# Kernel optimization log

Measured on AMD Instinct MI355X. Metric: run time of the kernel, lower is better.

The kernel has to match this reference:

```python
import jax, jax.numpy as jnp
import numpy as np
from jax import lax

NMS_RADIUS = 4
THRESHOLD = 0.005
BORDER = 4
MAX_KP = 1024


def _max_pool(x, r):
    # torch max_pool2d pads with -inf; reduce_window 'SAME' pads with init value.
    w = 2 * r + 1
    return lax.reduce_window(x, -jnp.inf, lax.max, (1, w, w), (1, 1, 1), 'SAME')


def simple_nms(scores, radius):
    zeros = jnp.zeros_like(scores)
    max_mask = scores == _max_pool(scores, radius)
    for _ in range(2):
        supp_mask = _max_pool(max_mask.astype(scores.dtype), radius) > 0
        supp_scores = jnp.where(supp_mask, zeros, scores)
        new_max_mask = supp_scores == _max_pool(supp_scores, radius)
        max_mask = max_mask | (new_max_mask & ~supp_mask)
    return jnp.where(max_mask, scores, zeros)


def sample_descriptors(kp, desc, s):
    """Bilinear grid_sample (align_corners=True, zero padding) + L2 normalize.
    kp: [B,N,2] (x,y) full-resolution pixel coords; desc: [B,C,h,w]."""
    b, c, h, w = desc.shape
    k = kp - s / 2 + 0.5
    gx = k[..., 0] / (w * s - 1) * 2.0 - 1.0
    gy = k[..., 1] / (h * s - 1) * 2.0 - 1.0
    x = (gx + 1.0) * 0.5 * (w - 1)  # align_corners=True mapping
    y = (gy + 1.0) * 0.5 * (h - 1)
    x0 = jnp.floor(x); y0 = jnp.floor(y)
    wx1 = x - x0; wy1 = y - y0
    x0i = x0.astype(jnp.int32); y0i = y0.astype(jnp.int32)

    def tap(d_b, xi, yi):  # d_b [C,h,w]; xi,yi [N] -> [C,N], zero outside
        v = ((xi >= 0) & (xi < w) & (yi >= 0) & (yi < h)).astype(d_b.dtype)
        g = d_b[:, jnp.clip(yi, 0, h - 1), jnp.clip(xi, 0, w - 1)]
        return g * v

    def one(d_b, x0i, y0i, wx1, wy1):
        wx0 = 1.0 - wx1; wy0 = 1.0 - wy1
        return (tap(d_b, x0i, y0i) * (wx0 * wy0)
                + tap(d_b, x0i + 1, y0i) * (wx1 * wy0)
                + tap(d_b, x0i, y0i + 1) * (wx0 * wy1)
                + tap(d_b, x0i + 1, y0i + 1) * (wx1 * wy1))

    out = jax.vmap(one)(desc, x0i, y0i, wx1, wy1)  # [B,C,N]
    n = jnp.maximum(jnp.linalg.norm(out, axis=1, keepdims=True), 1e-12)
    return out / n


def conv1x1(w, b, x):  # Conv1d kernel_size=1: [O,I] @ [B,I,N]
    return jnp.einsum('oi,bin->bon', w, x) + b[None, :, None]


def setup_inputs() -> dict:
    key = jax.random.key(0)
    ks = jax.random.split(key, 13)
    B, H, W = 4, 480, 640
    inp = {
        'scores': jax.random.uniform(ks[0], (B, H, W), jnp.float32),
        'd1': jax.random.normal(ks[1], (B, 64, H // 2, W // 2), jnp.float32),
        'd2': jax.random.normal(ks[2], (B, 128, H // 4, W // 4), jnp.float32),
        'cDa': jax.random.normal(ks[3], (B, 256, H // 8, W // 8), jnp.float32),
        'd4': jax.random.normal(ks[4], (B, 256, H // 16, W // 16), jnp.float32),
        'lin0_w': jax.random.normal(ks[5], (256, 256), jnp.float32) / np.sqrt(256),
        'lin0_b': jax.random.normal(ks[6], (256,), jnp.float32) * 0.01,
        'lin1_w': jax.random.normal(ks[7], (128, 128), jnp.float32) / np.sqrt(128),
        'lin1_b': jax.random.normal(ks[8], (128,), jnp.float32) * 0.01,
        'lin2_w': jax.random.normal(ks[9], (64, 64), jnp.float32) / np.sqrt(64),
        'lin2_b': jax.random.normal(ks[10], (64,), jnp.float32) * 0.01,
        'merge_w': jax.random.normal(ks[11], (256, 704), jnp.float32) / np.sqrt(704),
        'merge_b': jax.random.normal(ks[12], (256,), jnp.float32) * 0.01,
    }
    return inp


def reference(scores, d1, d2, cDa, d4, lin0_w, lin0_b, lin1_w, lin1_b,
              lin2_w, lin2_b, merge_w, merge_b):
    B, H, W = scores.shape
    s = simple_nms(scores, NMS_RADIUS)
    ys, xs = jnp.meshgrid(jnp.arange(H), jnp.arange(W), indexing='ij')
    valid = (ys >= BORDER) & (ys < H - BORDER) & (xs >= BORDER) & (xs < W - BORDER)
    masked = jnp.where(valid[None] & (s > THRESHOLD), s, -1.0)
    top_scores, idx = lax.top_k(masked.reshape(B, -1), MAX_KP)
    kx = (idx % W).astype(jnp.float32)
    ky = (idx // W).astype(jnp.float32)
    kp = jnp.stack([kx, ky], axis=-1)  # [B,K,2] (x,y), i.e. torch.flip(k,[1])
    de1 = sample_descriptors(kp, d1, 2)    # [B,64,K]
    de2 = sample_descriptors(kp, d2, 4)    # [B,128,K]
    de3 = sample_descriptors(kp, cDa, 8)   # [B,256,K]
    de4 = sample_descriptors(kp, d4, 16)   # [B,256,K]
    de4 = conv1x1(lin0_w, lin0_b, de4)
    de2 = conv1x1(lin1_w, lin1_b, de2)
    de1 = conv1x1(lin2_w, lin2_b, de1)
    descriptors = conv1x1(merge_w, merge_b,
                          jnp.concatenate([de1, de2, de3, de4], axis=1))
    return kp, top_scores, descriptors
```

## Files before the change

### kernel.cpp

```cpp
#include <hip/hip_runtime.h>
#include <hip/hip_bf16.h>

#define B 4
#define H 480
#define W 640
#define HW (H*W)
#define BHW (B*H*W)
#define NKP 1024
#define THRESH 0.005f
#define CAP 16384
#define NCOL (B*NKP)
#define KTOT 704
#define KPB 4

typedef __attribute__((ext_vector_type(8))) short s8v;
typedef __attribute__((ext_vector_type(4))) float f4v;
typedef struct { float x, y; } __attribute__((aligned(4))) f2u;

__device__ __forceinline__ short f2bf(float f) {
    __hip_bfloat16 h = __float2bfloat16(f);
    return *(short*)&h;
}

__device__ __forceinline__ float max3f(float a, float b, float c) {
    return fmaxf(fmaxf(a, b), c);
}
#define MAX9(A, base, str) \
    max3f(max3f((A)[(base)], (A)[(base)+(str)], (A)[(base)+2*(str)]), \
          max3f((A)[(base)+3*(str)], (A)[(base)+4*(str)], (A)[(base)+5*(str)]), \
          max3f((A)[(base)+6*(str)], (A)[(base)+7*(str)], (A)[(base)+8*(str)]))

__global__ void fuse_all(const float* __restrict__ merge_w, const float* __restrict__ merge_b,
                         const float* __restrict__ lin0_w, const float* __restrict__ lin0_b,
                         const float* __restrict__ lin1_w, const float* __restrict__ lin1_b,
                         const float* __restrict__ lin2_w, const float* __restrict__ lin2_b,
                         short* __restrict__ Mw, float* __restrict__ biasf, int* __restrict__ cnt) {
    if (blockIdx.x == 704) {
        int o = threadIdx.x;
        if (o < 4) cnt[o * 64] = 0;
        float acc = merge_b[o];
        for (int k = 0; k < 64; ++k)  acc += merge_w[o * KTOT + k] * lin2_b[k];
        for (int k = 0; k < 128; ++k) acc += merge_w[o * KTOT + 64 + k] * lin1_b[k];
        for (int k = 0; k < 256; ++k) acc += merge_w[o * KTOT + 448 + k] * lin0_b[k];
        biasf[o] = acc;
        return;
    }
    int e = blockIdx.x * 256 + threadIdx.x;
    int o = e / KTOT;
    int j = e - o * KTOT;
    float acc = 0.0f;
    if (j < 64) {
        for (int k = 0; k < 64; ++k) acc += merge_w[o * KTOT + k] * lin2_w[k * 64 + j];
    } else if (j < 192) {
        int jj = j - 64;
        for (int k = 0; k < 128; ++k) acc += merge_w[o * KTOT + 64 + k] * lin1_w[k * 128 + jj];
    } else if (j < 448) {
        acc = merge_w[o * KTOT + j];
    } else {
        int jj = j - 448;
        for (int k = 0; k < 256; ++k) acc += merge_w[o * KTOT + 448 + k] * lin0_w[k * 256 + jj];
    }
    Mw[o * KTOT + j] = f2bf(acc);
}

__global__ __launch_bounds__(256) void nms1(const float* __restrict__ scores,
                                            float* __restrict__ mask) {
    __shared__ float tile[40][40];
    __shared__ float hm[40][32];
    int bz = blockIdx.z;
    int x0 = blockIdx.x * 32, y0 = blockIdx.y * 32;
    const float* sp = scores + bz * HW;
    for (int t = threadIdx.x; t < 1600; t += 256) {
        int ly = t / 40, lx = t - ly * 40;
        int gy = y0 - 4 + ly, gx = x0 - 4 + lx;
        tile[ly][lx] = (gy >= 0 && gy < H && gx >= 0 && gx < W) ? sp[gy * W + gx] : -INFINITY;
    }
    __syncthreads();
    for (int t = threadIdx.x; t < 1280; t += 256) {
        int ly = t >> 5, lx = t & 31;
        hm[ly][lx] = MAX9(&tile[ly][0], lx, 1);
    }
    __syncthreads();
    for (int t = threadIdx.x; t < 1024; t += 256) {
        int ly = t >> 5, lx = t & 31;
        float m = MAX9(&hm[0][0], ly * 32 + lx, 32);
        float s = tile[ly + 4][lx + 4];
        mask[bz * HW + (y0 + ly) * W + x0 + lx] = (s == m) ? 1.0f : 0.0f;
    }
}

__global__ __launch_bounds__(512) void nms2_compact(const float* __restrict__ scores,
                                                    const float* __restrict__ mask0,
                                                    unsigned long long* __restrict__ cand,
                                                    int* __restrict__ cnt) {
    __shared__ float Sm[56 * 56];
    __shared__ float Mm[64 * 64];
    __shared__ float Zm[56 * 56];
    __shared__ float Tm[64 * 56];
    __shared__ int lcnt, gbase;
    int bz = blockIdx.z;
    int x0 = blockIdx.x * 32, y0 = blockIdx.y * 32;
    const float* sp = scores + bz * HW;
    const float* mp = mask0 + bz * HW;
    if (threadIdx.x == 0) lcnt = 0;
    for (int t = threadIdx.x; t < 4096; t += 512) {
        int ly = t >> 6, lx = t & 63;
        int gy = y0 - 16 + ly, gx = x0 - 16 + lx;
        Mm[t] = (gy >= 0 && gy < H && gx >= 0 && gx < W) ? mp[gy * W + gx] : 0.0f;
    }
    for (int t = threadIdx.x; t < 3136; t += 512) {
        int i = t / 56, j = t - i * 56;
        int gy = y0 - 12 + i, gx = x0 - 12 + j;
        Sm[t] = (gy >= 0 && gy < H && gx >= 0 && gx < W) ? sp[gy * W + gx] : -1.0f;
    }
    __syncthreads();
    for (int t = threadIdx.x; t < 3584; t += 512) {
        int i = t / 56, c = t - i * 56;
        Tm[i * 56 + c] = MAX9(Mm, i * 64 + c, 1);
    }
    __syncthreads();
    for (int t = threadIdx.x; t < 3136; t += 512) {
        int i = t / 56, c = t - i * 56;
        float m = MAX9(Tm, i * 56 + c, 56);
        Zm[t] = (m > 0.0f) ? -1.0f : Sm[t];
    }
    __syncthreads();
    for (int t = threadIdx.x; t < 2688; t += 512) {
        int i = t / 48, c = t - i * 48;
        Tm[i * 56 + c] = MAX9(Zm, i * 56 + c, 1);
    }
    __syncthreads();
    for (int t = threadIdx.x; t < 2304; t += 512) {
        int r = t / 48, c = t - r * 48;
        float m = MAX9(Tm, r * 56 + c, 56);
        float Zc = Zm[(r + 4) * 56 + c + 4];
        int mi = (r + 8) * 64 + c + 8;
        bool nm = (Zc == m) && (Zc >= 0.0f);
        Mm[mi] = (Mm[mi] != 0.0f || nm) ? 1.0f : 0.0f;
    }
    __syncthreads();
    for (int t = threadIdx.x; t < 1920; t += 512) {
        int r = t / 40, c = t - r * 40;
        Tm[r * 56 + c] = MAX9(Mm, (r + 8) * 64 + c + 8, 1);
    }
    __syncthreads();
    for (int t = threadIdx.x; t < 1600; t += 512) {
        int r = t / 40, c = t - r * 40;
        float m = MAX9(Tm, r * 56 + c, 56);
        int zi = (r + 8) * 56 + c + 8;
        Zm[zi] = (m > 0.0f) ? -1.0f : Sm[zi];
    }
    __syncthreads();
    for (int t = threadIdx.x; t < 1280; t += 512) {
        int r = t / 32, c = t & 31;
        Tm[r * 56 + c] = MAX9(Zm, (r + 8) * 56 + c + 8, 1);
    }
    __syncthreads();
    unsigned long long keys[2];
    int nl = 0;
    #pragma unroll
    for (int q = 0; q < 2; ++q) {
        int t = threadIdx.x + q * 512;
        int r3 = t >> 5, c = t & 31;
        float m = MAX9(Tm, r3 * 56 + c, 56);
        float Zc = Zm[(r3 + 12) * 56 + c + 12];
        bool fin = (Mm[(r3 + 16) * 64 + c + 16] != 0.0f) || ((Zc == m) && (Zc >= 0.0f));
        int gy = y0 + r3, gx = x0 + c;
        float sc = Sm[(r3 + 12) * 56 + c + 12];
        if (fin && gy >= 4 && gy < H - 4 && gx >= 4 && gx < W - 4 && sc > THRESH) {
            unsigned r = (unsigned)(gy * W + gx);
            unsigned bits = __float_as_uint(sc) | 0x80000000u;
            keys[nl++] = ((unsigned long long)bits << 32) |
                         (unsigned long long)(0xFFFFFFFFu - r);
        }
    }
    int lpos = 0;
    if (nl) lpos = atomicAdd(&lcnt, nl);
    __syncthreads();
    if (threadIdx.x == 0) gbase = (lcnt > 0) ? atomicAdd(&cnt[bz * 64], lcnt) : 0;
    __syncthreads();
    for (int j = 0; j < nl; ++j) {
        int p = gbase + lpos + j;
        if (p < CAP) cand[(size_t)bz * CAP + p] = keys[j];
    }
}

__global__ __launch_bounds__(1024) void topk(const unsigned long long* __restrict__ cand,
                                             const int* __restrict__ cnt,
                                             float* __restrict__ out, int* __restrict__ fidx,
                                             int* __restrict__ perm) {
    __shared__ int hist[2048];
    __shared__ unsigned long long buf[4096];
    __shared__ int scnt, spiv1, spiv2, sabove;
    int b = blockIdx.x, tid = threadIdx.x;
    int m = cnt[b * 64]; if (m > CAP) m = CAP;
    const unsigned long long* cb = cand + (size_t)b * CAP;
    int target = (m < 1024) ? m : 1024;

    hist[tid] = 0; hist[tid + 1024] = 0;
    if (tid == 0) { scnt = 0; spiv1 = 2048; spiv2 = 0; sabove = 0; }
    __syncthreads();
    for (int i = tid; i < m; i += 1024)
        atomicAdd(&hist[(int)(cb[i] >> 53) & 0x7FF], 1);
    __syncthreads();
    for (int d = 1; d < 2048; d <<= 1) {
        int v0 = hist[tid] + ((tid + d < 2048) ? hist[tid + d] : 0);
        int v1 = hist[tid + 1024] + ((tid + 1024 + d < 2048) ? hist[tid + 1024 + d] : 0);
        __syncthreads();
        hist[tid] = v0; hist[tid + 1024] = v1;
        __syncthreads();
    }
    if (target > 0) {
        for (int t = tid; t < 2048; t += 1024) {
            int c = hist[t];
            int cn = (t < 2047) ? hist[t + 1] : 0;
            if (c >= target && cn < target) { spiv1 = t; sabove = cn; }
        }
    }
    __syncthreads();
    int piv1 = spiv1;
    int target2 = target - sabove;
    hist[tid] = 0; hist[tid + 1024] = 0;
    __syncthreads();
    for (int i = tid; i < m; i += 1024) {
        unsigned long long k = cb[i];
        if (((int)(k >> 53) & 0x7FF) == piv1)
            atomicAdd(&hist[(int)(k >> 42) & 0x7FF], 1);
    }
    __syncthreads();
    for (int d = 1; d < 2048; d <<= 1) {
        int v0 = hist[tid] + ((tid + d < 2048) ? hist[tid + d] : 0);
        int v1 = hist[tid + 1024] + ((tid + 1024 + d < 2048) ? hist[tid + 1024 + d] : 0);
        __syncthreads();
        hist[tid] = v0; hist[tid + 1024] = v1;
        __syncthreads();
    }
    if (target > 0) {
        for (int t = tid; t < 2048; t += 1024) {
            int c = hist[t];
            int cn = (t < 2047) ? hist[t + 1] : 0;
            if (c >= target2 && cn < target2) spiv2 = t;
        }
    }
    __syncthreads();
    int piv2 = spiv2;
    for (int i = tid; i < m; i += 1024) {
        unsigned long long k = cb[i];
        int b1 = (int)(k >> 53) & 0x7FF;
        bool sel = (target > 0) &&
                   (b1 > piv1 || (b1 == piv1 && (((int)(k >> 42) & 0x7FF) >= piv2)));
        if (sel) {
            int p = atomicAdd(&scnt, 1);
            if (p < 4096) buf[p] = k;
        }
    }
    __syncthreads();
    int sc_ = scnt; if (sc_ > 4096) sc_ = 4096;
    int ns = 1024; while (ns < sc_) ns <<= 1;
    for (int t = tid; t < ns; t += 1024) if (t >= sc_) buf[t] = 0ULL;
    __syncthreads();
    for (int k = 2; k <= ns; k <<= 1)
        for (int j = k >> 1; j > 0; j >>= 1) {
            __syncthreads();
            for (int t = tid; t < ns; t += 1024) {
                int ixj = t ^ j;
                if (ixj > t) {
                    unsigned long long a = buf[t], bb = buf[ixj];
                    if (((t & k) == 0) ? (a < bb) : (a > bb)) { buf[t] = bb; buf[ixj] = a; }
                }
            }
        }
    __syncthreads();
    unsigned long long key = buf[tid];
    float kx, ky, sc;
    unsigned idx;
    if (key != 0ULL) {
        unsigned ord = (unsigned)(key >> 32);
        sc = __uint_as_float(ord ^ 0x80000000u);
        idx = 0xFFFFFFFFu - (unsigned)(key & 0xFFFFFFFFu);
        kx = (float)(idx % W);
        ky = (float)(idx / W);
    } else {
        sc = -1.0f; idx = 0; kx = 0.0f; ky = 0.0f;
    }
    int bn = b * NKP + tid;
    out[bn * 2 + 0] = kx;
    out[bn * 2 + 1] = ky;
    out[B * NKP * 2 + bn] = sc;
    fidx[bn] = (int)idx;
    __syncthreads();
    unsigned* b32 = (unsigned*)buf;
    b32[tid] = (idx << 10) | (unsigned)tid;
    for (int k = 2; k <= 1024; k <<= 1)
        for (int j = k >> 1; j > 0; j >>= 1) {
            __syncthreads();
            int ixj = tid ^ j;
            if (ixj > tid) {
                unsigned a = b32[tid], bb = b32[ixj];
                if (((tid & k) == 0) ? (a > bb) : (a < bb)) { b32[tid] = bb; b32[ixj] = a; }
            }
        }
    __syncthreads();
    perm[b * NKP + tid] = (int)(b32[tid] & 1023u);
}

__global__ __launch_bounds__(704) void sample_all(const float* __restrict__ d1,
                                                  const float* __restrict__ d2,
                                                  const float* __restrict__ cDa,
                                                  const float* __restrict__ d4,
                                                  const int* __restrict__ fidx,
                                                  const int* __restrict__ perm,
                                                  short* __restrict__ X) {
    __shared__ float ssum[KPB][12];
    int c = threadIdx.x;
    int wid = c >> 6, lane = c & 63;
    int bid = blockIdx.x;
    int swz = ((bid & 7) << 7) | (bid >> 3);
    int b = swz >> 8;
    int g0 = (swz & 255) * KPB;

    const float* map; int h, w, s, C, cl;
    if (c < 64)       { map = d1;  h = 240; w = 320; s = 2;  cl = c;       C = 64; }
    else if (c < 192) { map = d2;  h = 120; w = 160; s = 4;  cl = c - 64;  C = 128; }
    else if (c < 448) { map = cDa; h = 60;  w = 80;  s = 8;  cl = c - 192; C = 256; }
    else              { map = d4;  h = 30;  w = 40;  s = 16; cl = c - 448; C = 256; }
    const float* plane = map + ((size_t)(b * C + cl)) * (h * w);

    int cols[KPB];
    float vals[KPB];
    float q0x[KPB], q0y[KPB], q1x[KPB], q1y[KPB];
    float ax[KPB], ay[KPB], bx[KPB], by[KPB];

    #pragma unroll
    for (int k = 0; k < KPB; ++k) {
        int col = (b << 10) | perm[(b << 10) + g0 + k];
        cols[k] = col;
        int idx = fidx[col];
        float kx = (float)(idx % W);
        float ky = (float)(idx / W);
        float kxs = kx - (float)s * 0.5f + 0.5f;
        float kys = ky - (float)s * 0.5f + 0.5f;
        float gx = kxs / (float)(w * s - 1) * 2.0f - 1.0f;
        float gy = kys / (float)(h * s - 1) * 2.0f - 1.0f;
        float x = (gx + 1.0f) * 0.5f * (float)(w - 1);
        float y = (gy + 1.0f) * 0.5f * (float)(h - 1);
        float x0f = floorf(x), y0f = floorf(y);
        int x0 = (int)x0f, y0 = (int)y0f;
        float wx1 = x - x0f, wy1 = y - y0f;
        float wx0 = 1.0f - wx1, wy0 = 1.0f - wy1;
        bool vx0 = (x0 >= 0) && (x0 < w);
        bool vx1 = (x0 + 1 >= 0) && (x0 + 1 < w);
        bool vy0 = (y0 >= 0) && (y0 < h);
        bool vy1 = (y0 + 1 >= 0) && (y0 + 1 < h);
        int xc0 = min(max(x0, 0), w - 1), xc1 = min(max(x0 + 1, 0), w - 1);
        int yc0 = min(max(y0, 0), h - 1), yc1 = min(max(y0 + 1, 0), h - 1);
        float w00 = (vx0 && vy0) ? wx0 * wy0 : 0.0f;
        float w01 = (vx1 && vy0) ? wx1 * wy0 : 0.0f;
        float w10 = (vx0 && vy1) ? wx0 * wy1 : 0.0f;
        float w11 = (vx1 && vy1) ? wx1 * wy1 : 0.0f;
        int xb = min(xc0, w - 2);
        float s0 = (xc0 == xb) ? 1.0f : 0.0f;
        float s1 = (xc1 == xb) ? 1.0f : 0.0f;
        ax[k] = w00 * s0 + w01 * s1;
        ay[k] = w00 * (1.0f - s0) + w01 * (1.0f - s1);
        bx[k] = w10 * s0 + w11 * s1;
        by[k] = w10 * (1.0f - s0) + w11 * (1.0f - s1);
        f2u q0 = *(const f2u*)(plane + yc0 * w + xb);
        f2u q1 = *(const f2u*)(plane + yc1 * w + xb);
        q0x[k] = q0.x; q0y[k] = q0.y;
        q1x[k] = q1.x; q1y[k] = q1.y;
    }
    #pragma unroll
    for (int k = 0; k < KPB; ++k)
        vals[k] = q0x[k] * ax[k] + q0y[k] * ay[k] + q1x[k] * bx[k] + q1y[k] * by[k];

    #pragma unroll
    for (int k = 0; k < KPB; ++k) {
        float r = vals[k] * vals[k];
        #pragma unroll
        for (int off = 32; off > 0; off >>= 1) r += __shfl_xor(r, off, 64);
        if (lane == 0) ssum[k][wid] = r;
    }
    __syncthreads();
    int wbeg, wcnt;
    if (c < 64)       { wbeg = 0; wcnt = 1; }
    else if (c < 192) { wbeg = 1; wcnt = 2; }
    else if (c < 448) { wbeg = 3; wcnt = 4; }
    else              { wbeg = 7; wcnt = 4; }
    #pragma unroll
    for (int k = 0; k < KPB; ++k) {
        float sum = 0.0f;
        for (int t = 0; t < wcnt; ++t) sum += ssum[k][wbeg + t];
        float denom = fmaxf(sqrtf(sum), 1e-12f);
        X[(size_t)cols[k] * KTOT + c] = f2bf(vals[k] / denom);
    }
}

__global__ __launch_bounds__(256) void gemm_mfma(const short* __restrict__ Mw,
                                                 const short* __restrict__ X,
                                                 const float* __restrict__ biasf,
                                                 float* __restrict__ out) {
    __shared__ short As[64 * 72];
    __shared__ short Bs[64 * 72];
    int tid = threadIdx.x;
    int lane = tid & 63, w = tid >> 6;
    int r = lane & 15, quad = lane >> 4;
    int rowBase = blockIdx.y * 64, colBase = blockIdx.x * 64;
    int sm = tid >> 2, skq = (tid & 3) << 4;

    const short* pa = Mw + (size_t)(rowBase + sm) * KTOT + skq;
    const short* pb = X + (size_t)(colBase + sm) * KTOT + skq;
    s8v a0 = *(const s8v*)(pa), a1 = *(const s8v*)(pa + 8);
    s8v b0 = *(const s8v*)(pb), b1 = *(const s8v*)(pb + 8);

    f4v acc[4];
    #pragma unroll
    for (int t = 0; t < 4; ++t) acc[t] = (f4v)0.0f;

    for (int kt = 0; kt < 11; ++kt) {
        __syncthreads();
        *(s8v*)&As[sm * 72 + skq + 0] = a0;
        *(s8v*)&As[sm * 72 + skq + 8] = a1;
        *(s8v*)&Bs[sm * 72 + skq + 0] = b0;
        *(s8v*)&Bs[sm * 72 + skq + 8] = b1;
        __syncthreads();
        if (kt < 10) {
            pa += 64; pb += 64;
            a0 = *(const s8v*)(pa); a1 = *(const s8v*)(pa + 8);
            b0 = *(const s8v*)(pb); b1 = *(const s8v*)(pb + 8);
        }
        #pragma unroll
        for (int kk = 0; kk < 2; ++kk) {
            int aoff = (w * 16 + r) * 72 + kk * 32 + quad * 8;
            s8v af = *(const s8v*)&As[aoff];
            #pragma unroll
            for (int t = 0; t < 4; ++t) {
                int boff = (t * 16 + r) * 72 + kk * 32 + quad * 8;
                s8v bf = *(const s8v*)&Bs[boff];
                acc[t] = __builtin_amdgcn_mfma_f32_16x16x32_bf16(af, bf, acc[t], 0, 0, 0);
            }
        }
    }
    #pragma unroll
    for (int t = 0; t < 4; ++t) {
        int colg = colBase + t * 16 + r;
        size_t obase = (size_t)(colg >> 10) * (256 * NKP) + (size_t)(colg & 1023);
        #pragma unroll
        for (int reg = 0; reg < 4; ++reg) {
            int row = rowBase + w * 16 + quad * 4 + reg;
            out[obase + (size_t)row * NKP] = acc[t][reg] + biasf[row];
        }
    }
}

extern "C" void kernel_launch(void* const* d_in, const int* in_sizes, int n_in,
                              void* d_out, int out_size, void* d_ws, size_t ws_size,
                              hipStream_t stream) {
    const float* scores  = (const float*)d_in[0];
    const float* d1      = (const float*)d_in[1];
    const float* d2      = (const float*)d_in[2];
    const float* cDa     = (const float*)d_in[3];
    const float* d4      = (const float*)d_in[4];
    const float* lin0_w  = (const float*)d_in[5];
    const float* lin0_b  = (const float*)d_in[6];
    const float* lin1_w  = (const float*)d_in[7];
    const float* lin1_b  = (const float*)d_in[8];
    const float* lin2_w  = (const float*)d_in[9];
    const float* lin2_b  = (const float*)d_in[10];
    const float* merge_w = (const float*)d_in[11];
    const float* merge_b = (const float*)d_in[12];
    float* out = (float*)d_out;

    char* ws = (char*)d_ws;
    float* MASK = (float*)ws;
    short* Xbuf = (short*)ws;
    unsigned long long* cand  = (unsigned long long*)(ws + 14745600);
    int* cnt                  = (int*)(ws + 15269888);
    int* fidx                 = (int*)(ws + 15401984);
    short* Mw                 = (short*)(ws + 15418368);
    float* biasf              = (float*)(ws + 16139264);
    int* perm                 = (int*)(ws + 16140288);

    dim3 tgrid(W / 32, H / 32, B);

    fuse_all<<<705, 256, 0, stream>>>(merge_w, merge_b, lin0_w, lin0_b, lin1_w, lin1_b,
                                      lin2_w, lin2_b, Mw, biasf, cnt);
    nms1<<<tgrid, 256, 0, stream>>>(scores, MASK);
    nms2_compact<<<tgrid, 512, 0, stream>>>(scores, MASK, cand, cnt);
    topk<<<B, 1024, 0, stream>>>(cand, cnt, out, fidx, perm);
    sample_all<<<(B * NKP) / KPB, KTOT, 0, stream>>>(d1, d2, cDa, d4, fidx, perm, Xbuf);
    gemm_mfma<<<dim3(NCOL / 64, 256 / 64), 256, 0, stream>>>(Mw, Xbuf, biasf, out + B * NKP * 3);
}
```

Baseline: 354.7 us.

## Restructure descriptor sampling: one wave per keypoint per map segment

The sampling kernel is remapped from 704-thread blocks (one thread per channel, four keypoints per block) to 256-thread blocks where each wave handles one keypoint for one descriptor map, with the map chosen by blockIdx.y. Each lane loads up to four channels strided by 64, so the L2 norm comes from a single wave shuffle reduction. This removes the shared-memory partial sums and the __syncthreads, and it replaces per-element division with one reciprocal multiply. In exchange the grid has more, smaller blocks, and the bilinear coordinate math is recomputed for every segment.

```diff
diff --git a/kernel.cpp b/kernel.cpp
--- a/kernel.cpp
+++ b/kernel.cpp
@@ -11,7 +11,6 @@
 #define CAP 16384
 #define NCOL (B*NKP)
 #define KTOT 704
-#define KPB 4
 
 typedef __attribute__((ext_vector_type(8))) short s8v;
 typedef __attribute__((ext_vector_type(4))) float f4v;
@@ -304,95 +303,91 @@
     perm[b * NKP + tid] = (int)(b32[tid] & 1023u);
 }
 
-__global__ __launch_bounds__(704) void sample_all(const float* __restrict__ d1,
+__global__ __launch_bounds__(256) void sample_all(const float* __restrict__ d1,
                                                   const float* __restrict__ d2,
                                                   const float* __restrict__ cDa,
                                                   const float* __restrict__ d4,
                                                   const int* __restrict__ fidx,
                                                   const int* __restrict__ perm,
                                                   short* __restrict__ X) {
-    __shared__ float ssum[KPB][12];
-    int c = threadIdx.x;
-    int wid = c >> 6, lane = c & 63;
+    int lane = threadIdx.x & 63;
+    int wv = threadIdx.x >> 6;
+    int seg = blockIdx.y;
     int bid = blockIdx.x;
     int swz = ((bid & 7) << 7) | (bid >> 3);
     int b = swz >> 8;
-    int g0 = (swz & 255) * KPB;
-
-    const float* map; int h, w, s, C, cl;
-    if (c < 64)       { map = d1;  h = 240; w = 320; s = 2;  cl = c;       C = 64; }
-    else if (c < 192) { map = d2;  h = 120; w = 160; s = 4;  cl = c - 64;  C = 128; }
-    else if (c < 448) { map = cDa; h = 60;  w = 80;  s = 8;  cl = c - 192; C = 256; }
-    else              { map = d4;  h = 30;  w = 40;  s = 16; cl = c - 448; C = 256; }
-    const float* plane = map + ((size_t)(b * C + cl)) * (h * w);
-
-    int cols[KPB];
-    float vals[KPB];
-    float q0x[KPB], q0y[KPB], q1x[KPB], q1y[KPB];
-    float ax[KPB], ay[KPB], bx[KPB], by[KPB];
-
-    #pragma unroll
-    for (int k = 0; k < KPB; ++k) {
-        int col = (b << 10) | perm[(b << 10) + g0 + k];
-        cols[k] = col;
-        int idx = fidx[col];
-        float kx = (float)(idx % W);
-        float ky = (float)(idx / W);
-        float kxs = kx - (float)s * 0.5f + 0.5f;
-        float kys = ky - (float)s * 0.5f + 0.5f;
-        float gx = kxs / (float)(w * s - 1) * 2.0f - 1.0f;
-        float gy = kys / (float)(h * s - 1) * 2.0f - 1.0f;
-        float x = (gx + 1.0f) * 0.5f * (float)(w - 1);
-        float y = (gy + 1.0f) * 0.5f * (float)(h - 1);
-        float x0f = floorf(x), y0f = floorf(y);
-        int x0 = (int)x0f, y0 = (int)y0f;
-        float wx1 = x - x0f, wy1 = y - y0f;
-        float wx0 = 1.0f - wx1, wy0 = 1.0f - wy1;
-        bool vx0 = (x0 >= 0) && (x0 < w);
-        bool vx1 = (x0 + 1 >= 0) && (x0 + 1 < w);
-        bool vy0 = (y0 >= 0) && (y0 < h);
-        bool vy1 = (y0 + 1 >= 0) && (y0 + 1 < h);
-        int xc0 = min(max(x0, 0), w - 1), xc1 = min(max(x0 + 1, 0), w - 1);
-        int yc0 = min(max(y0, 0), h - 1), yc1 = min(max(y0 + 1, 0), h - 1);
-        float w00 = (vx0 && vy0) ? wx0 * wy0 : 0.0f;
-        float w01 = (vx1 && vy0) ? wx1 * wy0 : 0.0f;
-        float w10 = (vx0 && vy1) ? wx0 * wy1 : 0.0f;
-        float w11 = (vx1 && vy1) ? wx1 * wy1 : 0.0f;
-        int xb = min(xc0, w - 2);
-        float s0 = (xc0 == xb) ? 1.0f : 0.0f;
-        float s1 = (xc1 == xb) ? 1.0f : 0.0f;
-        ax[k] = w00 * s0 + w01 * s1;
-        ay[k] = w00 * (1.0f - s0) + w01 * (1.0f - s1);
-        bx[k] = w10 * s0 + w11 * s1;
-        by[k] = w10 * (1.0f - s0) + w11 * (1.0f - s1);
-        f2u q0 = *(const f2u*)(plane + yc0 * w + xb);
-        f2u q1 = *(const f2u*)(plane + yc1 * w + xb);
-        q0x[k] = q0.x; q0y[k] = q0.y;
-        q1x[k] = q1.x; q1y[k] = q1.y;
-    }
-    #pragma unroll
-    for (int k = 0; k < KPB; ++k)
-        vals[k] = q0x[k] * ax[k] + q0y[k] * ay[k] + q1x[k] * bx[k] + q1y[k] * by[k];
-
-    #pragma unroll
-    for (int k = 0; k < KPB; ++k) {
-        float r = vals[k] * vals[k];
-        #pragma unroll
-        for (int off = 32; off > 0; off >>= 1) r += __shfl_xor(r, off, 64);
-        if (lane == 0) ssum[k][wid] = r;
-    }
-    __syncthreads();
-    int wbeg, wcnt;
-    if (c < 64)       { wbeg = 0; wcnt = 1; }
-    else if (c < 192) { wbeg = 1; wcnt = 2; }
-    else if (c < 448) { wbeg = 3; wcnt = 4; }
-    else              { wbeg = 7; wcnt = 4; }
-    #pragma unroll
-    for (int k = 0; k < KPB; ++k) {
-        float sum = 0.0f;
-        for (int t = 0; t < wcnt; ++t) sum += ssum[k][wbeg + t];
-        float denom = fmaxf(sqrtf(sum), 1e-12f);
-        X[(size_t)cols[k] * KTOT + c] = f2bf(vals[k] / denom);
+    int g0 = ((swz & 255) << 2) + wv;
+
+    const float* map; int h, w, s, C, base, nset;
+    if (seg == 0)      { map = d1;  h = 240; w = 320; s = 2;  C = 64;  base = 0;   nset = 1; }
+    else if (seg == 1) { map = d2;  h = 120; w = 160; s = 4;  C = 128; base = 64;  nset = 2; }
+    else if (seg == 2) { map = cDa; h = 60;  w = 80;  s = 8;  C = 256; base = 192; nset = 4; }
+    else               { map = d4;  h = 30;  w = 40;  s = 16; C = 256; base = 448; nset = 4; }
+
+    int col = (b << 10) | perm[(b << 10) + g0];
+    int idx = fidx[col];
+    float kx = (float)(idx % W);
+    float ky = (float)(idx / W);
+    float kxs = kx - (float)s * 0.5f + 0.5f;
+    float kys = ky - (float)s * 0.5f + 0.5f;
+    float gx = kxs / (float)(w * s - 1) * 2.0f - 1.0f;
+    float gy = kys / (float)(h * s - 1) * 2.0f - 1.0f;
+    float x = (gx + 1.0f) * 0.5f * (float)(w - 1);
+    float y = (gy + 1.0f) * 0.5f * (float)(h - 1);
+    float x0f = floorf(x), y0f = floorf(y);
+    int x0 = (int)x0f, y0 = (int)y0f;
+    float wx1 = x - x0f, wy1 = y - y0f;
+    float wx0 = 1.0f - wx1, wy0 = 1.0f - wy1;
+    bool vx0 = (x0 >= 0) && (x0 < w);
+    bool vx1 = (x0 + 1 >= 0) && (x0 + 1 < w);
+    bool vy0 = (y0 >= 0) && (y0 < h);
+    bool vy1 = (y0 + 1 >= 0) && (y0 + 1 < h);
+    int xc0 = min(max(x0, 0), w - 1), xc1 = min(max(x0 + 1, 0), w - 1);
+    int yc0 = min(max(y0, 0), h - 1), yc1 = min(max(y0 + 1, 0), h - 1);
+    float w00 = (vx0 && vy0) ? wx0 * wy0 : 0.0f;
+    float w01 = (vx1 && vy0) ? wx1 * wy0 : 0.0f;
+    float w10 = (vx0 && vy1) ? wx0 * wy1 : 0.0f;
+    float w11 = (vx1 && vy1) ? wx1 * wy1 : 0.0f;
+    int xb = min(xc0, w - 2);
+    float s0 = (xc0 == xb) ? 1.0f : 0.0f;
+    float s1 = (xc1 == xb) ? 1.0f : 0.0f;
+    float ax = w00 * s0 + w01 * s1;
+    float ay = w00 * (1.0f - s0) + w01 * (1.0f - s1);
+    float bx = w10 * s0 + w11 * s1;
+    float by = w10 * (1.0f - s0) + w11 * (1.0f - s1);
+
+    size_t hw = (size_t)(h * w);
+    const float* pb = map + ((size_t)b * C + lane) * hw;
+    size_t off0 = (size_t)yc0 * w + xb;
+    size_t off1 = (size_t)yc1 * w + xb;
+    size_t cstr = hw << 6;
+
+    f2u q0[4], q1[4];
+    #pragma unroll
+    for (int j = 0; j < 4; ++j) {
+        if (j < nset) {
+            const float* p = pb + (size_t)j * cstr;
+            q0[j] = *(const f2u*)(p + off0);
+            q1[j] = *(const f2u*)(p + off1);
+        }
+    }
+    float vals[4];
+    float r = 0.0f;
+    #pragma unroll
+    for (int j = 0; j < 4; ++j) {
+        if (j < nset) {
+            vals[j] = q0[j].x * ax + q0[j].y * ay + q1[j].x * bx + q1[j].y * by;
+            r += vals[j] * vals[j];
+        }
+    }
+    #pragma unroll
+    for (int off = 32; off > 0; off >>= 1) r += __shfl_xor(r, off, 64);
+    float denom = fmaxf(sqrtf(r), 1e-12f);
+    float inv = 1.0f / denom;
+    short* xp = X + (size_t)col * KTOT + base + lane;
+    #pragma unroll
+    for (int j = 0; j < 4; ++j) {
+        if (j < nset) xp[j * 64] = f2bf(vals[j] * inv);
     }
 }
 
@@ -488,6 +483,6 @@
     nms1<<<tgrid, 256, 0, stream>>>(scores, MASK);
     nms2_compact<<<tgrid, 512, 0, stream>>>(scores, MASK, cand, cnt);
     topk<<<B, 1024, 0, stream>>>(cand, cnt, out, fidx, perm);
-    sample_all<<<(B * NKP) / KPB, KTOT, 0, stream>>>(d1, d2, cDa, d4, fidx, perm, Xbuf);
+    sample_all<<<dim3(1024, 4), 256, 0, stream>>>(d1, d2, cDa, d4, fidx, perm, Xbuf);
     gemm_mfma<<<dim3(NCOL / 64, 256 / 64), 256, 0, stream>>>(Mw, Xbuf, biasf, out + B * NKP * 3);
 }
```

Result: no change. 353.4 us (-0.3%).
